# Kernel optimization log

Hardware: AMD Instinct MI355X
Metric: run time of the kernel (lower is better)

Reference implementation:

```python
import jax, jax.numpy as jnp
import numpy as np

B, A, U, S, E, H = 32768, 8, 64, 512, 128, 4
HYP = 256  # unused (two_hyper_layers=False)
COEF = 0.001
NEG = -99999999.0


def setup_inputs() -> dict:
    key = jax.random.key(0)
    ks = jax.random.split(key, 11)
    def lin(k, shape, fan_in):
        return jax.random.normal(k, shape, dtype=jnp.float32) * (1.0 / np.sqrt(fan_in))
    return {
        "agent_qs": jax.random.normal(ks[0], (B, A), dtype=jnp.float32),
        "states": jax.random.normal(ks[1], (B, S), dtype=jnp.float32),
        "actions": jax.random.randint(ks[2], (B, A), 0, 10, dtype=jnp.int64),
        "W_sel": lin(ks[3], (H, E, S), S),        # per-head selector extractor (no bias)
        "W_key": lin(ks[4], (H, E, U + 1), U + 1),  # per-head key extractor (no bias)
        "Wv1": lin(ks[5], (E, S), S),
        "bv1": jnp.zeros((E,), dtype=jnp.float32),
        "Wv2": lin(ks[6], (1, E), E),
        "bv2": jnp.zeros((1,), dtype=jnp.float32),
        "Wh": lin(ks[7], (H, S), S),              # hyper_w_head
        "bh": jnp.zeros((H,), dtype=jnp.float32),
    }


def reference(agent_qs, states, actions, W_sel, W_key, Wv1, bv1, Wv2, bv2, Wh, bh):
    b = states.shape[0]
    unit = states[:, : U * A].reshape(b, A, U)                     # [B,A,U]
    x = jnp.concatenate([unit, agent_qs[:, :, None]], axis=2)       # [B,A,U+1] (nonlinear)
    sel = jnp.einsum('bs,hes->bhe', states, W_sel)                  # all-head selectors
    keys = jnp.einsum('bau,heu->bhae', x, W_key)                    # all-head keys
    logits = jnp.einsum('bhe,bhae->bha', sel, keys)                 # attend_logits per head
    scaled = logits / np.float32(np.sqrt(E))
    dead = (actions == 0)[:, None, :]                               # mask_dead
    scaled = jnp.where(dead, NEG, scaled)
    weights = jax.nn.softmax(scaled, axis=2)                        # [B,H,A]
    v = jax.nn.relu(states @ Wv1.T + bv1) @ Wv2.T + bv2             # [B,1]
    w_head = jnp.abs(states @ Wh.T + bh)                            # [B,H] weighted_head
    head_attend = jnp.sum(weights * w_head[:, :, None], axis=1)     # [B,A]
    attend_mag_regs = COEF * jnp.sum(jnp.mean(logits ** 2, axis=(0, 2)))
    head_entropies = -jnp.mean(jnp.sum(jnp.log(weights + 1e-8) * weights, axis=2), axis=0)  # [H]
    return head_attend, v, attend_mag_regs, head_entropies
```

## Files before the change

kernel.cpp:

```cpp
#include <hip/hip_runtime.h>


typedef unsigned short u16;
typedef unsigned int u32;
typedef float f32x4 __attribute__((ext_vector_type(4)));
typedef unsigned int u32x4 __attribute__((ext_vector_type(4)));
typedef unsigned int u32x2 __attribute__((ext_vector_type(2)));
typedef __attribute__((address_space(1))) const u32 gu32;
typedef __attribute__((address_space(3))) u32 lu32;

#define NEGV -99999999.0f
#define CSTRIDE 424

__device__ __forceinline__ u16 f2bf(float f) {
  union { float f; u32 u; } v; v.f = f;
  u32 r = v.u + 0x7fffu + ((v.u >> 16) & 1u);
  return (u16)(r >> 16);
}
__device__ __forceinline__ float bfl(u32 w) { union { u32 u; float f; } v; v.u = w << 16; return v.f; }
__device__ __forceinline__ float bfh(u32 w) { union { u32 u; float f; } v; v.u = w & 0xffff0000u; return v.f; }

__device__ __forceinline__ void panel_store(u16* Wp, int p, int s, float v) {
  const int kt = s >> 5, c = (s >> 3) & 3, j = s & 7;
  Wp[kt * 12800 + p * 32 + ((c ^ ((p >> 1) & 3)) << 3) + j] = f2bf(v);
}

__global__ __launch_bounds__(256) void kprep(
    const float* __restrict__ Wsel, const float* __restrict__ Wkey,
    const float* __restrict__ Wv1, const float* __restrict__ Wh,
    u16* __restrict__ Wp, float* __restrict__ accs) {
  const int bid = blockIdx.x, t = threadIdx.x;
  if (bid < 128) {
    __shared__ float wsS[2048];
    __shared__ float wkS[8320];
    const int h = bid >> 5, s0 = (bid & 31) << 4;
    for (int i = t; i < 2048; i += 256)
      wsS[i] = Wsel[((size_t)h * 128 + (i >> 4)) * 512 + s0 + (i & 15)];
    for (int i = t; i < 8320; i += 256)
      wkS[i] = Wkey[(size_t)h * 8320 + i];
    __syncthreads();
    {
      const int u = t >> 2, sl0 = (t & 3) << 2;
      float a0 = 0.f, a1 = 0.f, a2 = 0.f, a3 = 0.f;
      for (int e = 0; e < 128; ++e) {
        const float k = wkS[e * 65 + u];
        const float* wr = wsS + e * 16 + sl0;
        a0 = fmaf(k, wr[0], a0); a1 = fmaf(k, wr[1], a1);
        a2 = fmaf(k, wr[2], a2); a3 = fmaf(k, wr[3], a3);
      }
      const int p = h * 64 + u, s = s0 + sl0;
      panel_store(Wp, p, s, a0);     panel_store(Wp, p, s + 1, a1);
      panel_store(Wp, p, s + 2, a2); panel_store(Wp, p, s + 3, a3);
    }
    if (t < 16) {
      float a = 0.f;
      for (int e = 0; e < 128; ++e)
        a = fmaf(wkS[e * 65 + 64], wsS[e * 16 + t], a);
      panel_store(Wp, 256 + h, s0 + t, a);
    }
  } else {
    if (bid == 128 && t < 16) accs[t] = 0.f;
    for (int row = 260 + (bid - 128); row < 400; row += 8) {
      for (int s = t; s < 512; s += 256) {
        float v = 0.f;
        if (row >= 264 && row < 392) v = Wv1[(row - 264) * 512 + s];
        else if (row >= 392 && row < 396) v = Wh[(row - 392) * 512 + s];
        panel_store(Wp, row, s, v);
      }
    }
  }
}

__device__ __forceinline__ void stageB(unsigned char* ldsB, const char* gB, int wid) {
#pragma unroll
  for (int i = 0; i < 4; ++i) {
    const int c = wid + (i << 3);
    if (c < 25)
      __builtin_amdgcn_global_load_lds((gu32*)(gB + c * 1024),
                                       (lu32*)(ldsB + c * 1024), 16, 0, 0);
  }
}

__device__ __forceinline__ void stageA8(unsigned char* dst, const float4& x) {
  u32x2 w;
  w[0] = (u32)f2bf(x.x) | ((u32)f2bf(x.y) << 16);
  w[1] = (u32)f2bf(x.z) | ((u32)f2bf(x.w) << 16);
  *(u32x2*)dst = w;
}

__device__ __forceinline__ void computeT(const unsigned char* buf, int wid, int c16,
                                         int slot, f32x4 acc[4][4]) {
  u32x4 af[4];
#pragma unroll
  for (int r = 0; r < 4; ++r)
    af[r] = *(const u32x4*)(buf + (r * 16 + c16) * 64 + slot * 16);
#pragma unroll
  for (int i = 0; i < 4; ++i) {
    const int f = wid + (i << 3);
    if (f < 25) {
      u32x4 bfr = *(const u32x4*)(buf + 4096 + (f * 16 + c16) * 64 + slot * 16);
#pragma unroll
      for (int r = 0; r < 4; ++r)
        asm("v_mfma_f32_16x16x32_bf16 %0, %1, %2, %0"
            : "+v"(acc[r][i]) : "v"(af[r]), "v"(bfr));
    }
  }
}

__global__ __launch_bounds__(512, 4) void kmain(
    const float* __restrict__ states, const float* __restrict__ agent_qs,
    const int* __restrict__ actions, const u16* __restrict__ Wp,
    const float* __restrict__ bv1, const float* __restrict__ Wv2,
    const float* __restrict__ bv2, const float* __restrict__ bh,
    float* __restrict__ out, float* __restrict__ accs) {
  __shared__ __align__(16) unsigned char smem[59392 + 160];
  unsigned char* const buf0 = smem;
  unsigned char* const buf1 = smem + 29696;
  u16* const Ctile = (u16*)smem;
  float* const red = (float*)(smem + 59392);

  const int tid = threadIdx.x;
  const int wid = tid >> 6;
  const int lane = tid & 63;
  const int b0 = blockIdx.x * 64;

  const f32x4 zf = {0.f, 0.f, 0.f, 0.f};
  f32x4 acc[4][4];
#pragma unroll
  for (int r = 0; r < 4; ++r)
#pragma unroll
    for (int i = 0; i < 4; ++i) acc[r][i] = zf;

  const int ar = tid >> 3, ac8 = tid & 7;
  const float* aG = states + (size_t)(b0 + ar) * 512 + ac8 * 4;
  const int aWoff = ar * 64 + (((ac8 >> 1) ^ ((ar >> 1) & 3)) << 4) + (ac8 & 1) * 8;

  const int c16 = lane & 15, sq = lane >> 4;
  const int slot = sq ^ ((c16 >> 1) & 3);
  const char* const wpB = (const char*)Wp + lane * 16;

  float4 ax = *(const float4*)(aG);
  stageA8(buf0 + aWoff, ax);
  stageB(buf0 + 4096, wpB, wid);
  ax = *(const float4*)(aG + 32);
  __syncthreads();

  for (int kt = 0; kt < 15; ++kt) {
    unsigned char* const sb = (kt & 1) ? buf0 : buf1;
    unsigned char* const cb = (kt & 1) ? buf1 : buf0;
    stageA8(sb + aWoff, ax);
    stageB(sb + 4096, wpB + (size_t)(kt + 1) * 25600, wid);
    if (kt < 14) ax = *(const float4*)(aG + (kt + 2) * 32);
    computeT(cb, wid, c16, slot, acc);
    __syncthreads();
  }
  computeT(buf1, wid, c16, slot, acc);
  __syncthreads();

  asm volatile("s_nop 7\n\ts_nop 7" :::);

#pragma unroll
  for (int r = 0; r < 4; ++r)
#pragma unroll
    for (int i = 0; i < 4; ++i) {
      const int f = wid + (i << 3);
      if (f < 25) {
        const int col = (f << 4) + c16;
        const int rowb = (r << 4) + (sq << 2);
#pragma unroll
        for (int j = 0; j < 4; ++j)
          Ctile[(rowb + j) * CSTRIDE + col] = f2bf(acc[r][i][j]);
      }
    }
  __syncthreads();

  const int r = (wid << 3) + (lane >> 3);
  const int q8 = lane & 7;
  const int b = b0 + r;
  const u16* crow = Ctile + r * CSTRIDE;
  const float* srow = states + (size_t)b * 512;

  float m[4][8];
#pragma unroll
  for (int h = 0; h < 4; ++h) {
    u32x4 w = *(const u32x4*)(crow + h * 64 + q8 * 8);
#pragma unroll
    for (int k = 0; k < 4; ++k) {
      m[h][2 * k] = bfl(w[k]); m[h][2 * k + 1] = bfh(w[k]);
    }
  }

  float lp[4][8];
#pragma unroll
  for (int h = 0; h < 4; ++h)
#pragma unroll
    for (int a = 0; a < 8; ++a) lp[h][a] = 0.f;

#pragma unroll
  for (int a = 0; a < 8; ++a) {
    const float* xp = srow + a * 64 + q8 * 8;
    float4 v0 = *(const float4*)(xp);
    float4 v1 = *(const float4*)(xp + 4);
    float xv[8] = {v0.x, v0.y, v0.z, v0.w, v1.x, v1.y, v1.z, v1.w};
#pragma unroll
    for (int h = 0; h < 4; ++h) {
      float s = 0.f;
#pragma unroll
      for (int j = 0; j < 8; ++j) s = fmaf(m[h][j], xv[j], s);
      lp[h][a] = s;
    }
  }
#pragma unroll
  for (int h = 0; h < 4; ++h)
#pragma unroll
    for (int a = 0; a < 8; ++a) {
      float v = lp[h][a];
      v += __shfl_xor(v, 1, 64);
      v += __shfl_xor(v, 2, 64);
      v += __shfl_xor(v, 4, 64);
      lp[h][a] = v;
    }
  float4 q0 = *(const float4*)(agent_qs + (size_t)b * 8);
  float4 q1 = *(const float4*)(agent_qs + (size_t)b * 8 + 4);
  float qv[8] = {q0.x, q0.y, q0.z, q0.w, q1.x, q1.y, q1.z, q1.w};
  u32x2 w64 = *(const u32x2*)(crow + 256);
  float m64[4] = {bfl(w64[0]), bfh(w64[0]), bfl(w64[1]), bfh(w64[1])};
#pragma unroll
  for (int h = 0; h < 4; ++h)
#pragma unroll
    for (int a = 0; a < 8; ++a) lp[h][a] = fmaf(m64[h], qv[a], lp[h][a]);

  float magp = 0.f;
  if (q8 == 0) {
#pragma unroll
    for (int h = 0; h < 4; ++h)
#pragma unroll
      for (int a = 0; a < 8; ++a) magp = fmaf(lp[h][a], lp[h][a], magp);
  }
  float bvv[16], wvv[16], cv[16];
#pragma unroll
  for (int g = 0; g < 4; ++g) {
    *(float4*)(bvv + g * 4) = *(const float4*)(bv1 + q8 * 16 + g * 4);
    *(float4*)(wvv + g * 4) = *(const float4*)(Wv2 + q8 * 16 + g * 4);
  }
#pragma unroll
  for (int g = 0; g < 2; ++g) {
    u32x4 wv = *(const u32x4*)(crow + 264 + q8 * 16 + g * 8);
#pragma unroll
    for (int k = 0; k < 4; ++k) {
      cv[g * 8 + 2 * k] = bfl(wv[k]); cv[g * 8 + 2 * k + 1] = bfh(wv[k]);
    }
  }
  float vp = 0.f;
#pragma unroll
  for (int e2 = 0; e2 < 16; ++e2)
    vp = fmaf(fmaxf(cv[e2] + bvv[e2], 0.f), wvv[e2], vp);
  vp += __shfl_xor(vp, 1, 64);
  vp += __shfl_xor(vp, 2, 64);
  vp += __shfl_xor(vp, 4, 64);

  int av[8];
  const int* ap = actions + (size_t)b * 8;
#pragma unroll
  for (int a = 0; a < 8; ++a) av[a] = ap[a];

  u32x2 ww = *(const u32x2*)(crow + 392);
  float whr[4] = {bfl(ww[0]), bfh(ww[0]), bfl(ww[1]), bfh(ww[1])};
  float4 bh4 = *(const float4*)(bh);
  float bhv[4] = {bh4.x, bh4.y, bh4.z, bh4.w};

  const float scale = 0.088388347648318447f;
  float att[8];
#pragma unroll
  for (int a = 0; a < 8; ++a) att[a] = 0.f;
  float entp[4];
#pragma unroll
  for (int h = 0; h < 4; ++h) {
    float whv = fabsf(whr[h] + bhv[h]);
    float sc[8];
#pragma unroll
    for (int a = 0; a < 8; ++a)
      sc[a] = (av[a] == 0) ? NEGV : lp[h][a] * scale;
    float mx = sc[0];
#pragma unroll
    for (int a = 1; a < 8; ++a) mx = fmaxf(mx, sc[a]);
    float ex[8];
    float sum = 0.f;
#pragma unroll
    for (int a = 0; a < 8; ++a) { ex[a] = __expf(sc[a] - mx); sum += ex[a]; }
    float inv = 1.f / sum;
    float ent = 0.f;
#pragma unroll
    for (int a = 0; a < 8; ++a) {
      float w = ex[a] * inv;
      att[a] = fmaf(w, whv, att[a]);
      ent = fmaf(w, __logf(w + 1e-8f), ent);
    }
    entp[h] = ent;
  }

  if (q8 == 0) {
    float4 o0 = {att[0], att[1], att[2], att[3]};
    float4 o1 = {att[4], att[5], att[6], att[7]};
    *(float4*)(out + (size_t)b * 8) = o0;
    *(float4*)(out + (size_t)b * 8 + 4) = o1;
    out[262144 + b] = vp + bv2[0];
  }

  float r0 = magp;
  float r1 = (q8 == 0) ? entp[0] : 0.f;
  float r2 = (q8 == 0) ? entp[1] : 0.f;
  float r3 = (q8 == 0) ? entp[2] : 0.f;
  float r4 = (q8 == 0) ? entp[3] : 0.f;
#pragma unroll
  for (int off = 1; off < 64; off <<= 1) {
    r0 += __shfl_xor(r0, off, 64);
    r1 += __shfl_xor(r1, off, 64);
    r2 += __shfl_xor(r2, off, 64);
    r3 += __shfl_xor(r3, off, 64);
    r4 += __shfl_xor(r4, off, 64);
  }
  if (lane == 0) {
    red[wid * 5 + 0] = r0; red[wid * 5 + 1] = r1; red[wid * 5 + 2] = r2;
    red[wid * 5 + 3] = r3; red[wid * 5 + 4] = r4;
  }
  __syncthreads();
  if (tid < 5) {
    float s = 0.f;
#pragma unroll
    for (int w = 0; w < 8; ++w) s += red[w * 5 + tid];
    atomicAdd(&accs[tid], s);
  }
  __syncthreads();
  if (tid == 0) {
    u32* cnt = (u32*)(accs + 8);
    if (atomicAdd(cnt, 1u) == 511u) {
      float a0 = atomicAdd(&accs[0], 0.f);
      float a1 = atomicAdd(&accs[1], 0.f);
      float a2 = atomicAdd(&accs[2], 0.f);
      float a3 = atomicAdd(&accs[3], 0.f);
      float a4 = atomicAdd(&accs[4], 0.f);
      out[294912] = 0.001f * a0 * (1.0f / 262144.0f);
      out[294913] = -a1 * (1.0f / 32768.0f);
      out[294914] = -a2 * (1.0f / 32768.0f);
      out[294915] = -a3 * (1.0f / 32768.0f);
      out[294916] = -a4 * (1.0f / 32768.0f);
    }
  }
}

extern "C" void kernel_launch(void* const* d_in, const int* in_sizes, int n_in,
                              void* d_out, int out_size, void* d_ws, size_t ws_size,
                              hipStream_t stream) {
  const float* agent_qs = (const float*)d_in[0];
  const float* states   = (const float*)d_in[1];
  const int*   actions  = (const int*)d_in[2];
  const float* Wsel = (const float*)d_in[3];
  const float* Wkey = (const float*)d_in[4];
  const float* Wv1  = (const float*)d_in[5];
  const float* bv1  = (const float*)d_in[6];
  const float* Wv2  = (const float*)d_in[7];
  const float* bv2  = (const float*)d_in[8];
  const float* Wh   = (const float*)d_in[9];
  const float* bh   = (const float*)d_in[10];
  float* out = (float*)d_out;
  float* accs = (float*)d_ws;
  u16* Wp = (u16*)((char*)d_ws + 64);

  hipLaunchKernelGGL(kprep, dim3(136), dim3(256), 0, stream,
                     Wsel, Wkey, Wv1, Wh, Wp, accs);
  hipLaunchKernelGGL(kmain, dim3(512), dim3(512), 0, stream,
                     states, agent_qs, actions, Wp, bv1, Wv2, bv2, bh, out, accs);
}
```

Baseline: 56.41 us.

## Load GEMM operands directly from global into registers, dropping LDS staging

Replaces the double-buffered LDS pipeline (global_load_lds for weights, converted bf16 A tiles written to shared memory, barriers per k-step) with direct per-lane global loads of A and B fragments into registers that feed the MFMA builtin. The weight panel is no longer swizzled, and the shared allocation shrinks because only the C tile is needed. This removes LDS traffic and the barrier after every k-step. In exchange, each of the 8 waves re-reads the same states rows from global/L2 and converts them to bf16 redundantly, and memory latency is now hidden only by unrolling and occupancy.

```diff
diff --git a/kernel.cpp b/kernel.cpp
--- a/kernel.cpp
+++ b/kernel.cpp
@@ -4,10 +4,9 @@
 typedef unsigned short u16;
 typedef unsigned int u32;
 typedef float f32x4 __attribute__((ext_vector_type(4)));
+typedef short s16x8 __attribute__((ext_vector_type(8)));
 typedef unsigned int u32x4 __attribute__((ext_vector_type(4)));
 typedef unsigned int u32x2 __attribute__((ext_vector_type(2)));
-typedef __attribute__((address_space(1))) const u32 gu32;
-typedef __attribute__((address_space(3))) u32 lu32;
 
 #define NEGV -99999999.0f
 #define CSTRIDE 424
@@ -21,8 +20,7 @@
 __device__ __forceinline__ float bfh(u32 w) { union { u32 u; float f; } v; v.u = w & 0xffff0000u; return v.f; }
 
 __device__ __forceinline__ void panel_store(u16* Wp, int p, int s, float v) {
-  const int kt = s >> 5, c = (s >> 3) & 3, j = s & 7;
-  Wp[kt * 12800 + p * 32 + ((c ^ ((p >> 1) & 3)) << 3) + j] = f2bf(v);
+  Wp[(s >> 5) * 12800 + p * 32 + (s & 31)] = f2bf(v);
 }
 
 __global__ __launch_bounds__(256) void kprep(
@@ -71,57 +69,20 @@
   }
 }
 
-__device__ __forceinline__ void stageB(unsigned char* ldsB, const char* gB, int wid) {
-#pragma unroll
-  for (int i = 0; i < 4; ++i) {
-    const int c = wid + (i << 3);
-    if (c < 25)
-      __builtin_amdgcn_global_load_lds((gu32*)(gB + c * 1024),
-                                       (lu32*)(ldsB + c * 1024), 16, 0, 0);
-  }
-}
-
-__device__ __forceinline__ void stageA8(unsigned char* dst, const float4& x) {
-  u32x2 w;
-  w[0] = (u32)f2bf(x.x) | ((u32)f2bf(x.y) << 16);
-  w[1] = (u32)f2bf(x.z) | ((u32)f2bf(x.w) << 16);
-  *(u32x2*)dst = w;
-}
-
-__device__ __forceinline__ void computeT(const unsigned char* buf, int wid, int c16,
-                                         int slot, f32x4 acc[4][4]) {
-  u32x4 af[4];
-#pragma unroll
-  for (int r = 0; r < 4; ++r)
-    af[r] = *(const u32x4*)(buf + (r * 16 + c16) * 64 + slot * 16);
-#pragma unroll
-  for (int i = 0; i < 4; ++i) {
-    const int f = wid + (i << 3);
-    if (f < 25) {
-      u32x4 bfr = *(const u32x4*)(buf + 4096 + (f * 16 + c16) * 64 + slot * 16);
-#pragma unroll
-      for (int r = 0; r < 4; ++r)
-        asm("v_mfma_f32_16x16x32_bf16 %0, %1, %2, %0"
-            : "+v"(acc[r][i]) : "v"(af[r]), "v"(bfr));
-    }
-  }
-}
-
 __global__ __launch_bounds__(512, 4) void kmain(
     const float* __restrict__ states, const float* __restrict__ agent_qs,
     const int* __restrict__ actions, const u16* __restrict__ Wp,
     const float* __restrict__ bv1, const float* __restrict__ Wv2,
     const float* __restrict__ bv2, const float* __restrict__ bh,
     float* __restrict__ out, float* __restrict__ accs) {
-  __shared__ __align__(16) unsigned char smem[59392 + 160];
-  unsigned char* const buf0 = smem;
-  unsigned char* const buf1 = smem + 29696;
+  __shared__ __align__(16) unsigned char smem[54272 + 160];
   u16* const Ctile = (u16*)smem;
-  float* const red = (float*)(smem + 59392);
+  float* const red = (float*)(smem + 54272);
 
   const int tid = threadIdx.x;
   const int wid = tid >> 6;
   const int lane = tid & 63;
+  const int c16 = lane & 15, sq = lane >> 4;
   const int b0 = blockIdx.x * 64;
 
   const f32x4 zf = {0.f, 0.f, 0.f, 0.f};
@@ -131,33 +92,44 @@
 #pragma unroll
     for (int i = 0; i < 4; ++i) acc[r][i] = zf;
 
-  const int ar = tid >> 3, ac8 = tid & 7;
-  const float* aG = states + (size_t)(b0 + ar) * 512 + ac8 * 4;
-  const int aWoff = ar * 64 + (((ac8 >> 1) ^ ((ar >> 1) & 3)) << 4) + (ac8 & 1) * 8;
-
-  const int c16 = lane & 15, sq = lane >> 4;
-  const int slot = sq ^ ((c16 >> 1) & 3);
-  const char* const wpB = (const char*)Wp + lane * 16;
-
-  float4 ax = *(const float4*)(aG);
-  stageA8(buf0 + aWoff, ax);
-  stageB(buf0 + 4096, wpB, wid);
-  ax = *(const float4*)(aG + 32);
-  __syncthreads();
-
-  for (int kt = 0; kt < 15; ++kt) {
-    unsigned char* const sb = (kt & 1) ? buf0 : buf1;
-    unsigned char* const cb = (kt & 1) ? buf1 : buf0;
-    stageA8(sb + aWoff, ax);
-    stageB(sb + 4096, wpB + (size_t)(kt + 1) * 25600, wid);
-    if (kt < 14) ax = *(const float4*)(aG + (kt + 2) * 32);
-    computeT(cb, wid, c16, slot, acc);
-    __syncthreads();
-  }
-  computeT(buf1, wid, c16, slot, acc);
-  __syncthreads();
-
-  asm volatile("s_nop 7\n\ts_nop 7" :::);
+  const float* aP[4];
+#pragma unroll
+  for (int r = 0; r < 4; ++r)
+    aP[r] = states + (size_t)(b0 + r * 16 + c16) * 512 + sq * 8;
+  const u16* bP[4];
+#pragma unroll
+  for (int i = 0; i < 4; ++i) {
+    const int f = wid + (i << 3);
+    bP[i] = Wp + ((f < 25 ? f : 0) * 16 + c16) * 32 + sq * 8;
+  }
+
+#pragma unroll 2
+  for (int kt = 0; kt < 16; ++kt) {
+    s16x8 bfr[4];
+#pragma unroll
+    for (int i = 0; i < 4; ++i)
+      if (wid + (i << 3) < 25)
+        bfr[i] = *(const s16x8*)(bP[i] + kt * 12800);
+    s16x8 af[4];
+#pragma unroll
+    for (int r = 0; r < 4; ++r) {
+      const float* p = aP[r] + kt * 32;
+      float4 x0 = *(const float4*)(p);
+      float4 x1 = *(const float4*)(p + 4);
+      af[r][0] = (short)f2bf(x0.x); af[r][1] = (short)f2bf(x0.y);
+      af[r][2] = (short)f2bf(x0.z); af[r][3] = (short)f2bf(x0.w);
+      af[r][4] = (short)f2bf(x1.x); af[r][5] = (short)f2bf(x1.y);
+      af[r][6] = (short)f2bf(x1.z); af[r][7] = (short)f2bf(x1.w);
+    }
+#pragma unroll
+    for (int i = 0; i < 4; ++i)
+      if (wid + (i << 3) < 25) {
+#pragma unroll
+        for (int r = 0; r < 4; ++r)
+          acc[r][i] = __builtin_amdgcn_mfma_f32_16x16x32_bf16(
+              af[r], bfr[i], acc[r][i], 0, 0, 0);
+      }
+  }
 
 #pragma unroll
   for (int r = 0; r < 4; ++r)
```

Result: slower. 142.7 us (+153.0%).
